# Kernel optimization log

Measured on AMD Instinct MI355X. Metric: run time of the kernel, lower is better.

The kernel has to match this reference:

```python
import jax, jax.numpy as jnp
import numpy as np
import math

N_HEADS = 16

def setup_inputs() -> dict:
    key = jax.random.key(0)
    k1, k2, k3 = jax.random.split(key, 3)
    B, S, D = 2, 2048, 1024
    x = jax.random.normal(k1, (B, S, D), dtype=jnp.float32)
    qkv = 0.01 * jax.random.normal(k2, (3 * D, D), dtype=jnp.float32)
    wo = 0.01 * jax.random.normal(k3, (D, D), dtype=jnp.float32)
    return {"x": x, "qkv": qkv, "wo": wo}

def reference(x, qkv, wo):
    B, S, D = x.shape
    H = N_HEADS
    dh = D // H
    QKV = x @ qkv.T                      # [B,S,3D]
    Q, K, V = jnp.split(QKV, 3, axis=-1)
    q = Q.reshape(B, S, H, dh).transpose(0, 2, 1, 3)  # [B,H,S,dh]
    k = K.reshape(B, S, H, dh).transpose(0, 2, 1, 3)
    v = V.reshape(B, S, H, dh).transpose(0, 2, 1, 3)
    scores = jnp.einsum('bhqd,bhkd->bhqk', q, k) / math.sqrt(float(dh))
    # Faithful to original: multiply by lower-triangular mask, then set
    # exact zeros to -inf (masked positions become 0 then -inf).
    mask = jnp.tril(jnp.ones((S, S), dtype=scores.dtype))
    scores = scores * mask[None, None, :, :]
    scores = jnp.where(scores == 0, -jnp.inf, scores)
    attn = jax.nn.softmax(scores, axis=-1)
    out = jnp.einsum('bhqk,bhkd->bhqd', attn, v)       # [B,H,S,dh]
    out = out.transpose(0, 2, 1, 3).reshape(B, S, D)
    return out @ wo.T
```

## Files before the change

### kernel.cpp

```cpp
#include <hip/hip_runtime.h>

typedef unsigned short u16;
typedef unsigned int u32;
typedef __bf16 bf16x8 __attribute__((ext_vector_type(8)));
typedef float f32x4 __attribute__((ext_vector_type(4)));
typedef u16 u16x4 __attribute__((ext_vector_type(4)));

#define GL2LDS16(g, l)                                                         \
    __builtin_amdgcn_global_load_lds(                                          \
        (__attribute__((address_space(1))) const void*)(g),                    \
        (__attribute__((address_space(3))) void*)(l), 16, 0, 0)

#define SYNC_VM(n) asm volatile("s_waitcnt vmcnt(" #n ")\ns_barrier" ::: "memory")
#define BAR()      asm volatile("s_barrier" ::: "memory")

__device__ __forceinline__ u16 f2bf(float f) {
    union { float f; u32 u; } x; x.f = f;
    u32 r = x.u + 0x7FFFu + ((x.u >> 16) & 1u);
    return (u16)(r >> 16);
}

__device__ __forceinline__ u32 pack2bf(float f0, float f1) {
    union { float f; u32 u; } a, b;
    a.f = f0; b.f = f1;
    return __builtin_amdgcn_perm(b.u + 0x8000u, a.u + 0x8000u, 0x07060302u);
}

__device__ __forceinline__ bf16x8 scale_frag(bf16x8 v) {
#pragma unroll
    for (int i = 0; i < 8; ++i) v[i] = (__bf16)((float)v[i] * 0.1803368801f);
    return v;
}

__global__ __launch_bounds__(256) void convert_all_kernel(const float* __restrict__ x,
                                                          const float* __restrict__ qkv,
                                                          const float* __restrict__ wo,
                                                          u16* __restrict__ out) {
    int i = (blockIdx.x * 256 + threadIdx.x) * 4;
    const float* src;
    int off;
    if (i < 4194304)      { src = x;   off = i; }
    else if (i < 7340032) { src = qkv; off = i - 4194304; }
    else                  { src = wo;  off = i - 7340032; }
    float4 v = *(const float4*)(src + off);
    u16x4 o;
    o.x = f2bf(v.x); o.y = f2bf(v.y); o.z = f2bf(v.z); o.w = f2bf(v.w);
    *(u16x4*)(out + i) = o;
}

template <int TM, bool OUT_BF16, bool FUSE_VT>
__global__ __launch_bounds__(256) void gemm_bt(const u16* __restrict__ A,
                                               const u16* __restrict__ B,
                                               void* __restrict__ Cout,
                                               u16* __restrict__ VtG,
                                               int M, int N, int K) {
    constexpr int MI = TM / 32;
    __shared__ u16 As[2][TM * 32];
    __shared__ u16 Bs[2][128 * 32];
    const int tid = threadIdx.x;
    const int w = tid >> 6, lane = tid & 63, ln = lane & 15, qd = lane >> 4;
    const int wr = w >> 1, wc = w & 1;
    const int m0 = blockIdx.y * TM, n0 = blockIdx.x * 128;

    const int srow = tid >> 2, scol = (tid & 3) * 8;
    const u16* Abase = A + (size_t)(m0 + srow) * K + scol;
    const u16* Bbase = B + (size_t)(n0 + srow) * K + scol;

    f32x4 acc[MI][4] = {};
    const int nsteps = K >> 5;

#pragma unroll
    for (int it = 0; it < TM / 64; ++it)
        GL2LDS16(Abase + (size_t)(it * 64) * K, &As[0][(tid + it * 256) * 8]);
#pragma unroll
    for (int it = 0; it < 2; ++it)
        GL2LDS16(Bbase + (size_t)(it * 64) * K, &Bs[0][(tid + it * 256) * 8]);

    for (int s = 0; s < nsteps; ++s) {
        const u16* Ab = As[s & 1];
        const u16* Bb = Bs[s & 1];
        if (s + 1 < nsteps) {
            const int nk = (s + 1) << 5;
            const int nb = (s + 1) & 1;
#pragma unroll
            for (int it = 0; it < TM / 64; ++it)
                GL2LDS16(Abase + (size_t)(it * 64) * K + nk, &As[nb][(tid + it * 256) * 8]);
#pragma unroll
            for (int it = 0; it < 2; ++it)
                GL2LDS16(Bbase + (size_t)(it * 64) * K + nk, &Bs[nb][(tid + it * 256) * 8]);
            if constexpr (TM == 128) SYNC_VM(4); else SYNC_VM(3);
        } else {
            SYNC_VM(0);
        }

        bf16x8 af[MI], bfr[4];
#pragma unroll
        for (int i = 0; i < MI; ++i)
            af[i] = *(const bf16x8*)&Ab[(wr * (TM / 2) + i * 16 + ln) * 32 + qd * 8];
#pragma unroll
        for (int j = 0; j < 4; ++j)
            bfr[j] = *(const bf16x8*)&Bb[(wc * 64 + j * 16 + ln) * 32 + qd * 8];
#pragma unroll
        for (int i = 0; i < MI; ++i)
#pragma unroll
            for (int j = 0; j < 4; ++j)
                acc[i][j] = __builtin_amdgcn_mfma_f32_16x16x32_bf16(af[i], bfr[j], acc[i][j], 0, 0, 0);
        BAR();
    }

    if (FUSE_VT && n0 >= 2048) {
        const int bq = m0 >> 11;
        const int sl = (m0 & 2047) + wr * (TM / 2) + qd * 4;
#pragma unroll
        for (int i = 0; i < MI; ++i)
#pragma unroll
            for (int j = 0; j < 4; ++j) {
                int d = n0 - 2048 + wc * 64 + j * 16 + ln;
                int vrow = (bq * 16 + (d >> 6)) * 64 + (d & 63);
                u16x4 ov;
                ov.x = f2bf(acc[i][j][0]); ov.y = f2bf(acc[i][j][1]);
                ov.z = f2bf(acc[i][j][2]); ov.w = f2bf(acc[i][j][3]);
                *(u16x4*)&VtG[(size_t)vrow * 2048 + sl + i * 16] = ov;
            }
        return;
    }

#pragma unroll
    for (int i = 0; i < MI; ++i)
#pragma unroll
        for (int j = 0; j < 4; ++j)
#pragma unroll
            for (int r = 0; r < 4; ++r) {
                int row = m0 + wr * (TM / 2) + i * 16 + qd * 4 + r;
                int col = n0 + wc * 64 + j * 16 + ln;
                float v = acc[i][j][r];
                if constexpr (OUT_BF16)
                    ((u16*)Cout)[(size_t)row * N + col] = f2bf(v);
                else
                    ((float*)Cout)[(size_t)row * N + col] = v;
            }
}

__global__ __launch_bounds__(256) void attn_kernel(const u16* __restrict__ QKV,
                                                   const u16* __restrict__ VtG,
                                                   u16* __restrict__ AO) {
    __shared__ u16 Ks[2][64 * 64];
    __shared__ u16 Vts[2][64 * 64];
    __shared__ u16 Pls[4][16 * 64];

    const int tid = threadIdx.x;
    const int w = tid >> 6, lane = tid & 63, ln = lane & 15, qd = lane >> 4;
    const int b = blockIdx.z, h = blockIdx.y;
    const int qtA = blockIdx.x;
    const int qtB = 31 - qtA;
    const int XA = qtA * 64 + w * 16, XB = qtB * 64 + w * 16;
    const int myqA = XA + ln, myqB = XB + ln;
    const int bh = b * 16 + h;
    const int swz = ln & 7;
    const int nch = qtB + 1;

    const int sr0 = tid >> 3;
    const int sg = (tid & 7) ^ (sr0 & 7);
    const u16* ksrc = QKV + (size_t)(b * 2048 + sr0) * 3072 + 1024 + h * 64 + sg * 8;
    const u16* vsrc = VtG + (size_t)(bh * 64 + sr0) * 2048 + sg * 8;

    GL2LDS16(ksrc, &Ks[0][tid * 8]);
    GL2LDS16(ksrc + (size_t)32 * 3072, &Ks[0][tid * 8 + 2048]);
    GL2LDS16(vsrc, &Vts[0][tid * 8]);
    GL2LDS16(vsrc + (size_t)32 * 2048, &Vts[0][tid * 8 + 2048]);

    const u16* qpA = QKV + (size_t)(b * 2048 + myqA) * 3072 + h * 64;
    const u16* qpB = QKV + (size_t)(b * 2048 + myqB) * 3072 + h * 64;
    bf16x8 qfA0 = scale_frag(*(const bf16x8*)(qpA + qd * 8));
    bf16x8 qfA1 = scale_frag(*(const bf16x8*)(qpA + 32 + qd * 8));
    bf16x8 qfB0 = scale_frag(*(const bf16x8*)(qpB + qd * 8));
    bf16x8 qfB1 = scale_frag(*(const bf16x8*)(qpB + 32 + qd * 8));

    f32x4 oA[4] = {}, oB[4] = {};
    float lA = 0.f, lB = 0.f;
    u16* Pw = Pls[w];

    for (int c = 0; c < nch; ++c) {
        if (c + 1 < nch) {
            const int k1 = (c + 1) * 64;
            const int nb = (c + 1) & 1;
            GL2LDS16(ksrc + (size_t)k1 * 3072, &Ks[nb][tid * 8]);
            GL2LDS16(ksrc + (size_t)(k1 + 32) * 3072, &Ks[nb][tid * 8 + 2048]);
            GL2LDS16(vsrc + k1, &Vts[nb][tid * 8]);
            GL2LDS16(vsrc + k1 + 32 * 2048, &Vts[nb][tid * 8 + 2048]);
            SYNC_VM(4);
        } else {
            SYNC_VM(0);
        }
        const u16* Kb = Ks[c & 1];
        const u16* Vb = Vts[c & 1];
        const bool actA = (c <= qtA);

        f32x4 sA[4], sB[4];
#pragma unroll
        for (int kt = 0; kt < 4; ++kt) {
            const u16* kr = Kb + (kt * 16 + ln) * 64;
            bf16x8 kf0 = *(const bf16x8*)(kr + ((qd ^ swz) * 8));
            bf16x8 kf1 = *(const bf16x8*)(kr + (((qd + 4) ^ swz) * 8));
            f32x4 z = {0.f, 0.f, 0.f, 0.f};
            z = __builtin_amdgcn_mfma_f32_16x16x32_bf16(kf0, qfB0, z, 0, 0, 0);
            z = __builtin_amdgcn_mfma_f32_16x16x32_bf16(kf1, qfB1, z, 0, 0, 0);
            sB[kt] = z;
            if (actA) {
                f32x4 y = {0.f, 0.f, 0.f, 0.f};
                y = __builtin_amdgcn_mfma_f32_16x16x32_bf16(kf0, qfA0, y, 0, 0, 0);
                y = __builtin_amdgcn_mfma_f32_16x16x32_bf16(kf1, qfA1, y, 0, 0, 0);
                sA[kt] = y;
            }
        }

        if (c == qtB) {
#pragma unroll
            for (int kt = 0; kt < 4; ++kt)
#pragma unroll
                for (int r = 0; r < 4; ++r) {
                    int key = c * 64 + kt * 16 + qd * 4 + r;
                    if (key > myqB) sB[kt][r] = -1e30f;
                }
        }
#pragma unroll
        for (int kt = 0; kt < 4; ++kt) {
            float p0 = exp2f(sB[kt][0]), p1 = exp2f(sB[kt][1]);
            float p2 = exp2f(sB[kt][2]), p3 = exp2f(sB[kt][3]);
            lB += (p0 + p1) + (p2 + p3);
            uint2 pk = {pack2bf(p0, p1), pack2bf(p2, p3)};
            int g = kt * 2 + (qd >> 1);
            *(uint2*)&Pw[ln * 64 + ((g ^ swz) * 8) + (qd & 1) * 4] = pk;
        }
        bf16x8 pfB0 = *(const bf16x8*)&Pw[ln * 64 + ((qd ^ swz) * 8)];
        bf16x8 pfB1 = *(const bf16x8*)&Pw[ln * 64 + (((qd + 4) ^ swz) * 8)];

        bf16x8 pfA0, pfA1;
        if (actA) {
            if (c == qtA) {
#pragma unroll
                for (int kt = 0; kt < 4; ++kt)
#pragma unroll
                    for (int r = 0; r < 4; ++r) {
                        int key = c * 64 + kt * 16 + qd * 4 + r;
                        if (key > myqA) sA[kt][r] = -1e30f;
                    }
            }
#pragma unroll
            for (int kt = 0; kt < 4; ++kt) {
                float p0 = exp2f(sA[kt][0]), p1 = exp2f(sA[kt][1]);
                float p2 = exp2f(sA[kt][2]), p3 = exp2f(sA[kt][3]);
                lA += (p0 + p1) + (p2 + p3);
                uint2 pk = {pack2bf(p0, p1), pack2bf(p2, p3)};
                int g = kt * 2 + (qd >> 1);
                *(uint2*)&Pw[ln * 64 + ((g ^ swz) * 8) + (qd & 1) * 4] = pk;
            }
            pfA0 = *(const bf16x8*)&Pw[ln * 64 + ((qd ^ swz) * 8)];
            pfA1 = *(const bf16x8*)&Pw[ln * 64 + (((qd + 4) ^ swz) * 8)];
        }

#pragma unroll
        for (int dt = 0; dt < 4; ++dt) {
            const u16* vr = Vb + (dt * 16 + ln) * 64;
            bf16x8 vf0 = *(const bf16x8*)(vr + ((qd ^ swz) * 8));
            bf16x8 vf1 = *(const bf16x8*)(vr + (((qd + 4) ^ swz) * 8));
            oB[dt] = __builtin_amdgcn_mfma_f32_16x16x32_bf16(vf0, pfB0, oB[dt], 0, 0, 0);
            oB[dt] = __builtin_amdgcn_mfma_f32_16x16x32_bf16(vf1, pfB1, oB[dt], 0, 0, 0);
            if (actA) {
                oA[dt] = __builtin_amdgcn_mfma_f32_16x16x32_bf16(vf0, pfA0, oA[dt], 0, 0, 0);
                oA[dt] = __builtin_amdgcn_mfma_f32_16x16x32_bf16(vf1, pfA1, oA[dt], 0, 0, 0);
            }
        }
        BAR();
    }

    lA += __shfl_xor(lA, 16); lA += __shfl_xor(lA, 32);
    lB += __shfl_xor(lB, 16); lB += __shfl_xor(lB, 32);
    float invA = 1.0f / lA, invB = 1.0f / lB;
#pragma unroll
    for (int dt = 0; dt < 4; ++dt) {
        uint2 ovA = {pack2bf(oA[dt][0] * invA, oA[dt][1] * invA),
                     pack2bf(oA[dt][2] * invA, oA[dt][3] * invA)};
        *(uint2*)&AO[(size_t)(b * 2048 + myqA) * 1024 + h * 64 + dt * 16 + qd * 4] = ovA;
        uint2 ovB = {pack2bf(oB[dt][0] * invB, oB[dt][1] * invB),
                     pack2bf(oB[dt][2] * invB, oB[dt][3] * invB)};
        *(uint2*)&AO[(size_t)(b * 2048 + myqB) * 1024 + h * 64 + dt * 16 + qd * 4] = ovB;
    }
}

extern "C" void kernel_launch(void* const* d_in, const int* in_sizes, int n_in,
                              void* d_out, int out_size, void* d_ws, size_t ws_size,
                              hipStream_t stream) {
    const float* x   = (const float*)d_in[0];
    const float* qkv = (const float*)d_in[1];
    const float* wo  = (const float*)d_in[2];
    float* out = (float*)d_out;

    char* ws = (char*)d_ws;
    u16* xb    = (u16*)(ws + 0);
    u16* qkvb  = (u16*)(ws + 8388608);
    u16* wob   = (u16*)(ws + 14680064);
    u16* QKVo  = (u16*)(ws + 16777216);
    u16* AO    = (u16*)(ws + 41943040);
    u16* VtG   = (u16*)(ws + 50331648);

    convert_all_kernel<<<8192, 256, 0, stream>>>(x, qkv, wo, xb);

    gemm_bt<128, true, true><<<dim3(24, 32), 256, 0, stream>>>(xb, qkvb, QKVo, VtG,
                                                               4096, 3072, 1024);

    attn_kernel<<<dim3(16, 16, 2), 256, 0, stream>>>(QKVo, VtG, AO);

    gemm_bt<64, false, false><<<dim3(8, 64), 256, 0, stream>>>(AO, wob, out, nullptr,
                                                               4096, 1024, 1024);
}
```

Baseline: 186.1 us.

## Split causal attention into 32-row wave tiles with two-wave blocks

The attention kernel now launches 128-thread blocks, twice as many as before. Each wave owns one 32-query tile, and the two waves in a block take a low and a high tile (t and 63-t) that share the K/V stream. Previously each wave carried two 16-row tiles from the A/B pair with an active-flag branch. The change also swaps exp2f for raw v_exp_f32 and raises wave priority around the MFMA sections. The aim is finer-grained scheduling and shorter softmax code. The risk is that the low-tile wave idles at barriers while the high-tile wave keeps working, and that v_exp_f32 skips exp2f's edge-case handling.

Result: no change. 185.8 us (-0.1%).

```diff
diff --git a/kernel.cpp b/kernel.cpp
--- a/kernel.cpp
+++ b/kernel.cpp
@@ -24,6 +24,12 @@
     union { float f; u32 u; } a, b;
     a.f = f0; b.f = f1;
     return __builtin_amdgcn_perm(b.u + 0x8000u, a.u + 0x8000u, 0x07060302u);
+}
+
+__device__ __forceinline__ float fast_exp2(float x) {
+    float r;
+    asm("v_exp_f32 %0, %1" : "=v"(r) : "v"(x));
+    return r;
 }
 
 __device__ __forceinline__ bf16x8 scale_frag(bf16x8 v) {
@@ -141,36 +147,39 @@
             }
 }
 
-__global__ __launch_bounds__(256) void attn_kernel(const u16* __restrict__ QKV,
+__global__ __launch_bounds__(128) void attn_kernel(const u16* __restrict__ QKV,
                                                    const u16* __restrict__ VtG,
                                                    u16* __restrict__ AO) {
     __shared__ u16 Ks[2][64 * 64];
     __shared__ u16 Vts[2][64 * 64];
-    __shared__ u16 Pls[4][16 * 64];
+    __shared__ u16 Pls[2][16 * 64];
 
     const int tid = threadIdx.x;
     const int w = tid >> 6, lane = tid & 63, ln = lane & 15, qd = lane >> 4;
     const int b = blockIdx.z, h = blockIdx.y;
-    const int qtA = blockIdx.x;
-    const int qtB = 31 - qtA;
-    const int XA = qtA * 64 + w * 16, XB = qtB * 64 + w * 16;
-    const int myqA = XA + ln, myqB = XB + ln;
+    const int t = blockIdx.x;
+    const int tH = 63 - t;
+    const int tile = (w == 0) ? tH : t;
+    const int q0 = tile * 32 + ln;
+    const int q1 = q0 + 16;
     const int bh = b * 16 + h;
     const int swz = ln & 7;
-    const int nch = qtB + 1;
+    const int nchH = (tH >> 1) + 1;
+    const int mynch = (tile >> 1) + 1;
 
     const int sr0 = tid >> 3;
     const int sg = (tid & 7) ^ (sr0 & 7);
     const u16* ksrc = QKV + (size_t)(b * 2048 + sr0) * 3072 + 1024 + h * 64 + sg * 8;
     const u16* vsrc = VtG + (size_t)(bh * 64 + sr0) * 2048 + sg * 8;
 
-    GL2LDS16(ksrc, &Ks[0][tid * 8]);
-    GL2LDS16(ksrc + (size_t)32 * 3072, &Ks[0][tid * 8 + 2048]);
-    GL2LDS16(vsrc, &Vts[0][tid * 8]);
-    GL2LDS16(vsrc + (size_t)32 * 2048, &Vts[0][tid * 8 + 2048]);
-
-    const u16* qpA = QKV + (size_t)(b * 2048 + myqA) * 3072 + h * 64;
-    const u16* qpB = QKV + (size_t)(b * 2048 + myqB) * 3072 + h * 64;
+#pragma unroll
+    for (int i = 0; i < 4; ++i) {
+        GL2LDS16(ksrc + (size_t)(i * 16) * 3072, &Ks[0][tid * 8 + i * 1024]);
+        GL2LDS16(vsrc + (size_t)(i * 16) * 2048, &Vts[0][tid * 8 + i * 1024]);
+    }
+
+    const u16* qpA = QKV + (size_t)(b * 2048 + q0) * 3072 + h * 64;
+    const u16* qpB = QKV + (size_t)(b * 2048 + q1) * 3072 + h * 64;
     bf16x8 qfA0 = scale_frag(*(const bf16x8*)(qpA + qd * 8));
     bf16x8 qfA1 = scale_frag(*(const bf16x8*)(qpA + 32 + qd * 8));
     bf16x8 qfB0 = scale_frag(*(const bf16x8*)(qpB + qd * 8));
@@ -180,96 +189,87 @@
     float lA = 0.f, lB = 0.f;
     u16* Pw = Pls[w];
 
-    for (int c = 0; c < nch; ++c) {
-        if (c + 1 < nch) {
+    for (int c = 0; c < nchH; ++c) {
+        if (c + 1 < nchH) {
             const int k1 = (c + 1) * 64;
             const int nb = (c + 1) & 1;
-            GL2LDS16(ksrc + (size_t)k1 * 3072, &Ks[nb][tid * 8]);
-            GL2LDS16(ksrc + (size_t)(k1 + 32) * 3072, &Ks[nb][tid * 8 + 2048]);
-            GL2LDS16(vsrc + k1, &Vts[nb][tid * 8]);
-            GL2LDS16(vsrc + k1 + 32 * 2048, &Vts[nb][tid * 8 + 2048]);
-            SYNC_VM(4);
+#pragma unroll
+            for (int i = 0; i < 4; ++i) {
+                GL2LDS16(ksrc + (size_t)(k1 + i * 16) * 3072, &Ks[nb][tid * 8 + i * 1024]);
+                GL2LDS16(vsrc + k1 + (size_t)(i * 16) * 2048, &Vts[nb][tid * 8 + i * 1024]);
+            }
+            SYNC_VM(8);
         } else {
             SYNC_VM(0);
         }
-        const u16* Kb = Ks[c & 1];
-        const u16* Vb = Vts[c & 1];
-        const bool actA = (c <= qtA);
-
-        f32x4 sA[4], sB[4];
-#pragma unroll
-        for (int kt = 0; kt < 4; ++kt) {
-            const u16* kr = Kb + (kt * 16 + ln) * 64;
-            bf16x8 kf0 = *(const bf16x8*)(kr + ((qd ^ swz) * 8));
-            bf16x8 kf1 = *(const bf16x8*)(kr + (((qd + 4) ^ swz) * 8));
-            f32x4 z = {0.f, 0.f, 0.f, 0.f};
-            z = __builtin_amdgcn_mfma_f32_16x16x32_bf16(kf0, qfB0, z, 0, 0, 0);
-            z = __builtin_amdgcn_mfma_f32_16x16x32_bf16(kf1, qfB1, z, 0, 0, 0);
-            sB[kt] = z;
-            if (actA) {
-                f32x4 y = {0.f, 0.f, 0.f, 0.f};
-                y = __builtin_amdgcn_mfma_f32_16x16x32_bf16(kf0, qfA0, y, 0, 0, 0);
-                y = __builtin_amdgcn_mfma_f32_16x16x32_bf16(kf1, qfA1, y, 0, 0, 0);
-                sA[kt] = y;
-            }
-        }
-
-        if (c == qtB) {
-#pragma unroll
-            for (int kt = 0; kt < 4; ++kt)
-#pragma unroll
-                for (int r = 0; r < 4; ++r) {
-                    int key = c * 64 + kt * 16 + qd * 4 + r;
-                    if (key > myqB) sB[kt][r] = -1e30f;
-                }
-        }
-#pragma unroll
-        for (int kt = 0; kt < 4; ++kt) {
-            float p0 = exp2f(sB[kt][0]), p1 = exp2f(sB[kt][1]);
-            float p2 = exp2f(sB[kt][2]), p3 = exp2f(sB[kt][3]);
-            lB += (p0 + p1) + (p2 + p3);
-            uint2 pk = {pack2bf(p0, p1), pack2bf(p2, p3)};
-            int g = kt * 2 + (qd >> 1);
-            *(uint2*)&Pw[ln * 64 + ((g ^ swz) * 8) + (qd & 1) * 4] = pk;
-        }
-        bf16x8 pfB0 = *(const bf16x8*)&Pw[ln * 64 + ((qd ^ swz) * 8)];
-        bf16x8 pfB1 = *(const bf16x8*)&Pw[ln * 64 + (((qd + 4) ^ swz) * 8)];
-
-        bf16x8 pfA0, pfA1;
-        if (actA) {
-            if (c == qtA) {
+
+        if (c < mynch) {
+            const u16* Kb = Ks[c & 1];
+            const u16* Vb = Vts[c & 1];
+
+            f32x4 sA[4], sB[4];
+            __builtin_amdgcn_s_setprio(1);
+#pragma unroll
+            for (int kt = 0; kt < 4; ++kt) {
+                const u16* kr = Kb + (kt * 16 + ln) * 64;
+                bf16x8 kf0 = *(const bf16x8*)(kr + ((qd ^ swz) * 8));
+                bf16x8 kf1 = *(const bf16x8*)(kr + (((qd + 4) ^ swz) * 8));
+                f32x4 zA = {0.f, 0.f, 0.f, 0.f}, zB = {0.f, 0.f, 0.f, 0.f};
+                zA = __builtin_amdgcn_mfma_f32_16x16x32_bf16(kf0, qfA0, zA, 0, 0, 0);
+                zA = __builtin_amdgcn_mfma_f32_16x16x32_bf16(kf1, qfA1, zA, 0, 0, 0);
+                zB = __builtin_amdgcn_mfma_f32_16x16x32_bf16(kf0, qfB0, zB, 0, 0, 0);
+                zB = __builtin_amdgcn_mfma_f32_16x16x32_bf16(kf1, qfB1, zB, 0, 0, 0);
+                sA[kt] = zA; sB[kt] = zB;
+            }
+            __builtin_amdgcn_s_setprio(0);
+
+            if (c == mynch - 1) {
 #pragma unroll
                 for (int kt = 0; kt < 4; ++kt)
 #pragma unroll
                     for (int r = 0; r < 4; ++r) {
                         int key = c * 64 + kt * 16 + qd * 4 + r;
-                        if (key > myqA) sA[kt][r] = -1e30f;
+                        if (key > q0) sA[kt][r] = -1e30f;
+                        if (key > q1) sB[kt][r] = -1e30f;
                     }
             }
+
 #pragma unroll
             for (int kt = 0; kt < 4; ++kt) {
-                float p0 = exp2f(sA[kt][0]), p1 = exp2f(sA[kt][1]);
-                float p2 = exp2f(sA[kt][2]), p3 = exp2f(sA[kt][3]);
+                float p0 = fast_exp2(sA[kt][0]), p1 = fast_exp2(sA[kt][1]);
+                float p2 = fast_exp2(sA[kt][2]), p3 = fast_exp2(sA[kt][3]);
                 lA += (p0 + p1) + (p2 + p3);
                 uint2 pk = {pack2bf(p0, p1), pack2bf(p2, p3)};
                 int g = kt * 2 + (qd >> 1);
                 *(uint2*)&Pw[ln * 64 + ((g ^ swz) * 8) + (qd & 1) * 4] = pk;
             }
-            pfA0 = *(const bf16x8*)&Pw[ln * 64 + ((qd ^ swz) * 8)];
-            pfA1 = *(const bf16x8*)&Pw[ln * 64 + (((qd + 4) ^ swz) * 8)];
-        }
-
-#pragma unroll
-        for (int dt = 0; dt < 4; ++dt) {
-            const u16* vr = Vb + (dt * 16 + ln) * 64;
-            bf16x8 vf0 = *(const bf16x8*)(vr + ((qd ^ swz) * 8));
-            bf16x8 vf1 = *(const bf16x8*)(vr + (((qd + 4) ^ swz) * 8));
-            oB[dt] = __builtin_amdgcn_mfma_f32_16x16x32_bf16(vf0, pfB0, oB[dt], 0, 0, 0);
-            oB[dt] = __builtin_amdgcn_mfma_f32_16x16x32_bf16(vf1, pfB1, oB[dt], 0, 0, 0);
-            if (actA) {
+            bf16x8 pfA0 = *(const bf16x8*)&Pw[ln * 64 + ((qd ^ swz) * 8)];
+            bf16x8 pfA1 = *(const bf16x8*)&Pw[ln * 64 + (((qd + 4) ^ swz) * 8)];
+
+#pragma unroll
+            for (int kt = 0; kt < 4; ++kt) {
+                float p0 = fast_exp2(sB[kt][0]), p1 = fast_exp2(sB[kt][1]);
+                float p2 = fast_exp2(sB[kt][2]), p3 = fast_exp2(sB[kt][3]);
+                lB += (p0 + p1) + (p2 + p3);
+                uint2 pk = {pack2bf(p0, p1), pack2bf(p2, p3)};
+                int g = kt * 2 + (qd >> 1);
+                *(uint2*)&Pw[ln * 64 + ((g ^ swz) * 8) + (qd & 1) * 4] = pk;
+            }
+            bf16x8 pfB0 = *(const bf16x8*)&Pw[ln * 64 + ((qd ^ swz) * 8)];
+            bf16x8 pfB1 = *(const bf16x8*)&Pw[ln * 64 + (((qd + 4) ^ swz) * 8)];
+
+            __builtin_amdgcn_s_setprio(1);
+#pragma unroll
+            for (int dt = 0; dt < 4; ++dt) {
+                const u16* vr = Vb + (dt * 16 + ln) * 64;
+                bf16x8 vf0 = *(const bf16x8*)(vr + ((qd ^ swz) * 8));
+                bf16x8 vf1 = *(const bf16x8*)(vr + (((qd + 4) ^ swz) * 8));
                 oA[dt] = __builtin_amdgcn_mfma_f32_16x16x32_bf16(vf0, pfA0, oA[dt], 0, 0, 0);
                 oA[dt] = __builtin_amdgcn_mfma_f32_16x16x32_bf16(vf1, pfA1, oA[dt], 0, 0, 0);
-            }
+                oB[dt] = __builtin_amdgcn_mfma_f32_16x16x32_bf16(vf0, pfB0, oB[dt], 0, 0, 0);
+                oB[dt] = __builtin_amdgcn_mfma_f32_16x16x32_bf16(vf1, pfB1, oB[dt], 0, 0, 0);
+            }
+            __builtin_amdgcn_s_setprio(0);
         }
         BAR();
     }
@@ -281,10 +281,10 @@
     for (int dt = 0; dt < 4; ++dt) {
         uint2 ovA = {pack2bf(oA[dt][0] * invA, oA[dt][1] * invA),
                      pack2bf(oA[dt][2] * invA, oA[dt][3] * invA)};
-        *(uint2*)&AO[(size_t)(b * 2048 + myqA) * 1024 + h * 64 + dt * 16 + qd * 4] = ovA;
+        *(uint2*)&AO[(size_t)(b * 2048 + q0) * 1024 + h * 64 + dt * 16 + qd * 4] = ovA;
         uint2 ovB = {pack2bf(oB[dt][0] * invB, oB[dt][1] * invB),
                      pack2bf(oB[dt][2] * invB, oB[dt][3] * invB)};
-        *(uint2*)&AO[(size_t)(b * 2048 + myqB) * 1024 + h * 64 + dt * 16 + qd * 4] = ovB;
+        *(uint2*)&AO[(size_t)(b * 2048 + q1) * 1024 + h * 64 + dt * 16 + qd * 4] = ovB;
     }
 }
 
@@ -309,7 +309,7 @@
     gemm_bt<128, true, true><<<dim3(24, 32), 256, 0, stream>>>(xb, qkvb, QKVo, VtG,
                                                                4096, 3072, 1024);
 
-    attn_kernel<<<dim3(16, 16, 2), 256, 0, stream>>>(QKVo, VtG, AO);
+    attn_kernel<<<dim3(32, 16, 2), 128, 0, stream>>>(QKVo, VtG, AO);
 
     gemm_bt<64, false, false><<<dim3(8, 64), 256, 0, stream>>>(AO, wob, out, nullptr,
                                                                4096, 1024, 1024);
```
